# Performance work log

Measured on AMD Instinct MI355X. Metric: run time of the kernel, lower is better.

## Reference

```python
import jax, jax.numpy as jnp
import numpy as np

N = 50000
IN_F = 256
HID = 32
HEADS = 4
NEG_SLOPE = 0.2


def _gat_layer(x, edge_index, W, a_src, a_dst, bias):
    # x: [N, Fin]; W: [Fin, H*C]; a_src/a_dst: [H, C]; bias: [H*C]
    n = x.shape[0]
    H, C = a_src.shape
    h = (x @ W).reshape(n, H, C)                     # [N, H, C]
    alpha_src = jnp.einsum('nhc,hc->nh', h, a_src)   # [N, H]
    alpha_dst = jnp.einsum('nhc,hc->nh', h, a_dst)   # [N, H]
    src, dst = edge_index[0], edge_index[1]
    logits = alpha_src[src] + alpha_dst[dst]         # [E, H]
    logits = jax.nn.leaky_relu(logits, negative_slope=NEG_SLOPE)
    # segment softmax over edges grouped by destination node
    seg_max = jax.ops.segment_max(logits, dst, num_segments=n)
    seg_max = jnp.where(jnp.isfinite(seg_max), seg_max, 0.0)
    e = jnp.exp(logits - seg_max[dst])               # [E, H]
    denom = jax.ops.segment_sum(e, dst, num_segments=n)  # [N, H]
    attn = e / (denom[dst] + 1e-16)                  # [E, H]
    msg = h[src] * attn[:, :, None]                  # [E, H, C]
    out = jax.ops.segment_sum(msg, dst, num_segments=n)  # [N, H, C]
    return out.reshape(n, H * C) + bias


def _add_self_loops(edge_index, n):
    # PyG GATConv default add_self_loops=True
    loops = jnp.arange(n, dtype=edge_index.dtype)
    return jnp.concatenate([edge_index, jnp.stack([loops, loops])], axis=1)


def setup_inputs() -> dict:
    key = jax.random.key(0)
    ks = jax.random.split(key, 10)
    x = jax.random.normal(ks[0], (N, IN_F), dtype=jnp.float32)
    edge_index = jax.random.randint(ks[1], (2, 800000), 0, N, dtype=jnp.int64)
    d1 = HEADS * HID
    s1 = 1.0 / np.sqrt(IN_F)
    W1 = jax.random.normal(ks[2], (IN_F, d1), dtype=jnp.float32) * s1
    a_src1 = jax.random.normal(ks[3], (HEADS, HID), dtype=jnp.float32) * 0.1
    a_dst1 = jax.random.normal(ks[4], (HEADS, HID), dtype=jnp.float32) * 0.1
    b1 = jnp.zeros((d1,), dtype=jnp.float32)
    s2 = 1.0 / np.sqrt(d1)
    W2 = jax.random.normal(ks[5], (d1, d1), dtype=jnp.float32) * s2
    a_src2 = jax.random.normal(ks[6], (HEADS, HID), dtype=jnp.float32) * 0.1
    a_dst2 = jax.random.normal(ks[7], (HEADS, HID), dtype=jnp.float32) * 0.1
    b2 = jnp.zeros((d1,), dtype=jnp.float32)
    return {"x": x, "edge_index": edge_index, "W1": W1, "a_src1": a_src1,
            "a_dst1": a_dst1, "b1": b1, "W2": W2, "a_src2": a_src2,
            "a_dst2": a_dst2, "b2": b2}


def reference(x, edge_index, W1, a_src1, a_dst1, b1, W2, a_src2, a_dst2, b2):
    # Inference mode: dropout layers are identity.
    ei = _add_self_loops(edge_index, x.shape[0])
    h = _gat_layer(x, ei, W1, a_src1, a_dst1, b1)
    h = jax.nn.elu(h)
    h = _gat_layer(h, ei, W2, a_src2, a_dst2, b2)
    return h
```

## Files before the change

kernel.cpp:

```cpp
#include <hip/hip_runtime.h>
#include <hip/hip_fp16.h>
#include <math.h>

#define HEADS 4
#define HID 32
#define D1 128
#define IN_FEAT 256
#define NEG_SLOPE 0.2f
#define CAP 64
#define AGG_NODES 8
#define NPASS 8
#define EPT 8

#define WTS_STRIDE_H 72
#define HTS_STRIDE_H 136
#define SMEM_BYTES (128 * 272)

typedef _Float16 half8 __attribute__((ext_vector_type(8)));
typedef float f32x4 __attribute__((ext_vector_type(4)));
typedef long long ll2 __attribute__((ext_vector_type(2)));

static inline int ceil_div(int a, int b) { return (a + b - 1) / b; }

static __device__ inline float2 unpack_h2(unsigned int v) {
    __half2 h = __builtin_bit_cast(__half2, v);
    return __half22float2(h);
}

static __device__ inline void fma_mix_lo(float& a, unsigned int h2, float w) {
    asm("v_fma_mix_f32 %0, %1, %2, %0 op_sel:[0,0,0] op_sel_hi:[1,0,0]"
        : "+v"(a) : "v"(h2), "v"(w));
}
static __device__ inline void fma_mix_hi(float& a, unsigned int h2, float w) {
    asm("v_fma_mix_f32 %0, %1, %2, %0 op_sel:[1,0,0] op_sel_hi:[1,0,0]"
        : "+v"(a) : "v"(h2), "v"(w));
}

__global__ void init_prep(const unsigned int* __restrict__ raw, int* __restrict__ flag,
                          const float* __restrict__ W1, _Float16* __restrict__ WT1,
                          const float* __restrict__ W2, _Float16* __restrict__ WT2,
                          int* __restrict__ cnt, int N) {
    int i = blockIdx.x * blockDim.x + threadIdx.x;
    if (i < N) cnt[i] = 0;
    if (i < IN_FEAT * D1) {
        int k = i >> 7, n = i & 127;
        WT1[(size_t)n * IN_FEAT + k] = (_Float16)W1[i];
    }
    if (i < D1 * D1) {
        int k = i >> 7, n = i & 127;
        WT2[(size_t)n * D1 + k] = (_Float16)W2[i];
    }
    if (blockIdx.x == 0 && threadIdx.x < 64) {
        unsigned int hi = raw[2 * threadIdx.x + 1];
        unsigned long long b = __ballot(hi != 0u);
        if (threadIdx.x == 0) *flag = (b == 0ULL) ? 1 : 0;
    }
}

__device__ void scatter_body(int sbid, const void* __restrict__ raw,
                             const int* __restrict__ flag,
                             int* __restrict__ cnt,
                             unsigned short* __restrict__ slots,
                             int E, int N) {
    const int e0 = (sbid * 256 + (int)threadIdx.x) * EPT;
    const bool wide = (*flag != 0);
    int s[EPT], d[EPT];
    bool val[EPT];
    if (e0 + EPT <= E) {
        if (wide) {
            const ll2* ps = (const ll2*)((const long long*)raw + e0);
            const ll2* pd = (const ll2*)((const long long*)raw + E + e0);
#pragma unroll
            for (int i = 0; i < EPT / 2; ++i) {
                ll2 a = ps[i], b = pd[i];
                s[2 * i] = (int)a[0]; s[2 * i + 1] = (int)a[1];
                d[2 * i] = (int)b[0]; d[2 * i + 1] = (int)b[1];
            }
        } else {
            const int4* ps = (const int4*)((const int*)raw + e0);
            const int4* pd = (const int4*)((const int*)raw + E + e0);
#pragma unroll
            for (int i = 0; i < EPT / 4; ++i) {
                int4 a = ps[i], b = pd[i];
                s[4 * i] = a.x; s[4 * i + 1] = a.y; s[4 * i + 2] = a.z; s[4 * i + 3] = a.w;
                d[4 * i] = b.x; d[4 * i + 1] = b.y; d[4 * i + 2] = b.z; d[4 * i + 3] = b.w;
            }
        }
#pragma unroll
        for (int i = 0; i < EPT; ++i) val[i] = true;
    } else {
#pragma unroll
        for (int i = 0; i < EPT; ++i) {
            int e = e0 + i;
            val[i] = (e < E);
            if (val[i]) {
                if (wide) { s[i] = (int)((const long long*)raw)[e]; d[i] = (int)((const long long*)raw)[E + e]; }
                else      { s[i] = ((const int*)raw)[e];            d[i] = ((const int*)raw)[E + e]; }
            } else { s[i] = 0; d[i] = -1; }
        }
    }

    const int range = (N + NPASS - 1) / NPASS;
    int lo = 0;
    for (int p = 0; p < NPASS; ++p, lo += range) {
        const int hi = lo + range;
#pragma unroll
        for (int i = 0; i < EPT; ++i) {
            if (val[i] && d[i] >= lo && d[i] < hi) {
                int pos = atomicAdd(&cnt[d[i]], 1);
                if (pos < CAP) slots[(size_t)d[i] * CAP + pos] = (unsigned short)s[i];
            }
        }
        __syncthreads();
    }
}

template <int AF16>
__device__ void gemm_body(char* smem, int bid, const void* __restrict__ Ain,
                          const _Float16* __restrict__ WT,
                          _Float16* __restrict__ Hout,
                          const float* __restrict__ a_src,
                          const float* __restrict__ a_dst,
                          float* __restrict__ asrc_out,
                          float* __restrict__ adst_out,
                          int M, int K) {
    const int tid = threadIdx.x;
    const int wave = tid >> 6, lane = tid & 63;
    const int quad = lane >> 4, l16 = lane & 15;
    const int row0 = bid * 128;
    const int m0 = min(row0 + wave * 32 + l16, M - 1);
    const int m1 = min(row0 + wave * 32 + 16 + l16, M - 1);
    const float*    Af = (const float*)Ain;
    const _Float16* Ah = (const _Float16*)Ain;
    const uint4* WTg = (const uint4*)WT;
    const int K8 = K >> 3;

    f32x4 acc[2][8];
#pragma unroll
    for (int r = 0; r < 2; ++r)
#pragma unroll
        for (int c = 0; c < 8; ++c) acc[r][c] = (f32x4){0.f, 0.f, 0.f, 0.f};

    for (int kb = 0; kb < K; kb += 64) {
        __syncthreads();
#pragma unroll
        for (int i = 0; i < 4; ++i) {
            int c = tid + i * 256;
            int n = c >> 3, j = c & 7;
            uint4 v = WTg[(size_t)n * K8 + (kb >> 3) + j];
            *(uint4*)(smem + n * 144 + j * 16) = v;
        }
        __syncthreads();
#pragma unroll
        for (int kc = 0; kc < 2; ++kc) {
            int k0 = kb + kc * 32 + quad * 8;
            half8 a0f, a1f;
            if (AF16) {
                a0f = *(const half8*)(Ah + (size_t)m0 * K + k0);
                a1f = *(const half8*)(Ah + (size_t)m1 * K + k0);
            } else {
                float4 x0 = *(const float4*)(Af + (size_t)m0 * K + k0);
                float4 x1 = *(const float4*)(Af + (size_t)m0 * K + k0 + 4);
                float4 y0 = *(const float4*)(Af + (size_t)m1 * K + k0);
                float4 y1 = *(const float4*)(Af + (size_t)m1 * K + k0 + 4);
                a0f[0] = (_Float16)x0.x; a0f[1] = (_Float16)x0.y;
                a0f[2] = (_Float16)x0.z; a0f[3] = (_Float16)x0.w;
                a0f[4] = (_Float16)x1.x; a0f[5] = (_Float16)x1.y;
                a0f[6] = (_Float16)x1.z; a0f[7] = (_Float16)x1.w;
                a1f[0] = (_Float16)y0.x; a1f[1] = (_Float16)y0.y;
                a1f[2] = (_Float16)y0.z; a1f[3] = (_Float16)y0.w;
                a1f[4] = (_Float16)y1.x; a1f[5] = (_Float16)y1.y;
                a1f[6] = (_Float16)y1.z; a1f[7] = (_Float16)y1.w;
            }
#pragma unroll
            for (int c = 0; c < 8; ++c) {
                half8 bf = *(const half8*)(smem + (c * 16 + l16) * 144 + kc * 64 + quad * 16);
                acc[0][c] = __builtin_amdgcn_mfma_f32_16x16x32_f16(a0f, bf, acc[0][c], 0, 0, 0);
                acc[1][c] = __builtin_amdgcn_mfma_f32_16x16x32_f16(a1f, bf, acc[1][c], 0, 0, 0);
            }
        }
    }

    __syncthreads();
    _Float16* hts = (_Float16*)smem;
#pragma unroll
    for (int r = 0; r < 2; ++r)
#pragma unroll
        for (int c = 0; c < 8; ++c)
#pragma unroll
            for (int g = 0; g < 4; ++g) {
                int row = wave * 32 + r * 16 + quad * 4 + g;
                hts[row * HTS_STRIDE_H + c * 16 + l16] = (_Float16)acc[r][c][g];
            }
    __syncthreads();

    const int r = tid >> 1;
    const int part = tid & 1;
    const int grow = row0 + r;
    const uint4* hrow = (const uint4*)(smem + r * 272 + part * 128);
    if (grow < M) {
        uint4* dv = (uint4*)(Hout + (size_t)grow * 128 + part * 64);
#pragma unroll
        for (int i = 0; i < 8; ++i) dv[i] = hrow[i];
    }
#pragma unroll
    for (int t = 0; t < 2; ++t) {
        int hh = part * 2 + t;
        const uint4* hv = (const uint4*)(smem + r * 272 + hh * 64);
        const float4* as4 = (const float4*)(a_src + hh * HID);
        const float4* ad4 = (const float4*)(a_dst + hh * HID);
        float ps = 0.f, pd = 0.f;
#pragma unroll
        for (int b = 0; b < 4; ++b) {
            uint4 u = hv[b];
            float2 f0 = unpack_h2(u.x), f1 = unpack_h2(u.y);
            float2 f2 = unpack_h2(u.z), f3 = unpack_h2(u.w);
            float4 s0 = as4[b * 2], s1 = as4[b * 2 + 1];
            float4 d0 = ad4[b * 2], d1 = ad4[b * 2 + 1];
            ps += f0.x * s0.x + f0.y * s0.y + f1.x * s0.z + f1.y * s0.w
                + f2.x * s1.x + f2.y * s1.y + f3.x * s1.z + f3.y * s1.w;
            pd += f0.x * d0.x + f0.y * d0.y + f1.x * d0.z + f1.y * d0.w
                + f2.x * d1.x + f2.y * d1.y + f3.x * d1.z + f3.y * d1.w;
        }
        if (grow < M) {
            asrc_out[grow * 4 + hh] = ps;
            adst_out[grow * 4 + hh] = pd;
        }
    }
}

template <int AF16>
__global__ __launch_bounds__(256) void gemm128(const void* __restrict__ Ain,
                                               const _Float16* __restrict__ WT,
                                               _Float16* __restrict__ Hout,
                                               const float* __restrict__ a_src,
                                               const float* __restrict__ a_dst,
                                               float* __restrict__ asrc_out,
                                               float* __restrict__ adst_out,
                                               int M, int K) {
    __shared__ __align__(16) char smem[SMEM_BYTES];
    gemm_body<AF16>(smem, blockIdx.x, Ain, WT, Hout, a_src, a_dst,
                    asrc_out, adst_out, M, K);
}

template <int AF16>
__global__ __launch_bounds__(256) void gemm128_scatter(const void* __restrict__ Ain,
                                                       const _Float16* __restrict__ WT,
                                                       _Float16* __restrict__ Hout,
                                                       const float* __restrict__ a_src,
                                                       const float* __restrict__ a_dst,
                                                       float* __restrict__ asrc_out,
                                                       float* __restrict__ adst_out,
                                                       int M, int K,
                                                       const void* __restrict__ raw,
                                                       const int* __restrict__ flag,
                                                       int* __restrict__ cnt,
                                                       unsigned short* __restrict__ slots,
                                                       int E, int Sg) {
    __shared__ __align__(16) char smem[SMEM_BYTES];
    if ((int)blockIdx.x < Sg) {
        scatter_body(blockIdx.x, raw, flag, cnt, slots, E, M);
        return;
    }
    gemm_body<AF16>(smem, blockIdx.x - Sg, Ain, WT, Hout, a_src, a_dst,
                    asrc_out, adst_out, M, K);
}

__global__ __launch_bounds__(256) void aggregate(const _Float16* __restrict__ hb,
                                                 const int* __restrict__ cnt,
                                                 const unsigned short* __restrict__ slots,
                                                 const float* __restrict__ asrc,
                                                 const float* __restrict__ adst,
                                                 const float* __restrict__ bias,
                                                 float* __restrict__ out32,
                                                 _Float16* __restrict__ out16,
                                                 int N, int apply_elu) {
    const int w = threadIdx.x >> 6;
    const int lane = threadIdx.x & 63;
    const int half = lane >> 5;
    const int hl = lane & 31;
    const int idx = w * 2 + half;
    const int node = blockIdx.x * AGG_NODES + idx;
    const bool live = (node < N);

    __shared__ float wsh[AGG_NODES][CAP][4];
    __shared__ int ssh[AGG_NODES][CAP];

    int cntE = 0, count = 1;
    if (live) {
        cntE = min(cnt[node], CAP - 1);
        count = cntE + 1;
    }
    const unsigned short* nslots = slots + (size_t)node * CAP;

    float4 ad4 = live ? *(const float4*)&adst[node * 4] : make_float4(0.f, 0.f, 0.f, 0.f);

    const bool v0 = live && (hl < count);
    const bool v1 = live && (hl + 32 < count);
    float lv0[4] = {-1e30f, -1e30f, -1e30f, -1e30f};
    float lv1[4] = {-1e30f, -1e30f, -1e30f, -1e30f};
    if (v0) {
        int src = (hl < cntE) ? (int)nslots[hl] : node;
        ssh[idx][hl] = src << 8;
        float4 as4 = *(const float4*)&asrc[src * 4];
        float t0 = as4.x + ad4.x, t1 = as4.y + ad4.y;
        float t2 = as4.z + ad4.z, t3 = as4.w + ad4.w;
        lv0[0] = t0 > 0.f ? t0 : NEG_SLOPE * t0;
        lv0[1] = t1 > 0.f ? t1 : NEG_SLOPE * t1;
        lv0[2] = t2 > 0.f ? t2 : NEG_SLOPE * t2;
        lv0[3] = t3 > 0.f ? t3 : NEG_SLOPE * t3;
    }
    if (v1) {
        int j = hl + 32;
        int src = (j < cntE) ? (int)nslots[j] : node;
        ssh[idx][j] = src << 8;
        float4 as4 = *(const float4*)&asrc[src * 4];
        float t0 = as4.x + ad4.x, t1 = as4.y + ad4.y;
        float t2 = as4.z + ad4.z, t3 = as4.w + ad4.w;
        lv1[0] = t0 > 0.f ? t0 : NEG_SLOPE * t0;
        lv1[1] = t1 > 0.f ? t1 : NEG_SLOPE * t1;
        lv1[2] = t2 > 0.f ? t2 : NEG_SLOPE * t2;
        lv1[3] = t3 > 0.f ? t3 : NEG_SLOPE * t3;
    }

    float m[4];
#pragma unroll
    for (int h = 0; h < 4; ++h) m[h] = fmaxf(lv0[h], lv1[h]);
#pragma unroll
    for (int off = 16; off >= 1; off >>= 1)
#pragma unroll
        for (int h = 0; h < 4; ++h)
            m[h] = fmaxf(m[h], __shfl_xor(m[h], off, 64));

    float e0[4], e1[4], sum[4];
#pragma unroll
    for (int h = 0; h < 4; ++h) {
        e0[h] = v0 ? __expf(lv0[h] - m[h]) : 0.f;
        e1[h] = v1 ? __expf(lv1[h] - m[h]) : 0.f;
        sum[h] = e0[h] + e1[h];
    }
#pragma unroll
    for (int off = 16; off >= 1; off >>= 1)
#pragma unroll
        for (int h = 0; h < 4; ++h)
            sum[h] += __shfl_xor(sum[h], off, 64);

    if (v0) {
        float4 w4;
        w4.x = e0[0] / (sum[0] + 1e-16f);
        w4.y = e0[1] / (sum[1] + 1e-16f);
        w4.z = e0[2] / (sum[2] + 1e-16f);
        w4.w = e0[3] / (sum[3] + 1e-16f);
        *(float4*)&wsh[idx][hl][0] = w4;
    }
    if (v1) {
        float4 w4;
        w4.x = e1[0] / (sum[0] + 1e-16f);
        w4.y = e1[1] / (sum[1] + 1e-16f);
        w4.z = e1[2] / (sum[2] + 1e-16f);
        w4.w = e1[3] / (sum[3] + 1e-16f);
        *(float4*)&wsh[idx][hl + 32][0] = w4;
    }
    __syncthreads();

    const int q = hl >> 4;
    const int sub = hl & 15;
    const int hh = sub >> 2;
    const char* hbase = (const char*)hb;
    const int sub16 = sub * 16;

    float acc[8];
#pragma unroll
    for (int i = 0; i < 8; ++i) acc[i] = 0.f;

#define LDROW(off) (*(const uint4*)(hbase + (unsigned)((off) + sub16)))
#define ROW_FMA(u, wt)                                   \
    do {                                                 \
        fma_mix_lo(acc[0], (u).x, (wt));                 \
        fma_mix_hi(acc[1], (u).x, (wt));                 \
        fma_mix_lo(acc[2], (u).y, (wt));                 \
        fma_mix_hi(acc[3], (u).y, (wt));                 \
        fma_mix_lo(acc[4], (u).z, (wt));                 \
        fma_mix_hi(acc[5], (u).z, (wt));                 \
        fma_mix_lo(acc[6], (u).w, (wt));                 \
        fma_mix_hi(acc[7], (u).w, (wt));                 \
    } while (0)

    if (live) {
        int j = q;
        if (j + 6 < count) {
            int o0 = ssh[idx][j], o1 = ssh[idx][j + 2], o2 = ssh[idx][j + 4], o3 = ssh[idx][j + 6];
            float w0 = wsh[idx][j][hh], w1 = wsh[idx][j + 2][hh];
            float w2 = wsh[idx][j + 4][hh], w3 = wsh[idx][j + 6][hh];
            uint4 u0 = LDROW(o0), u1 = LDROW(o1), u2 = LDROW(o2), u3 = LDROW(o3);
            for (j += 8; j + 6 < count; j += 8) {
                int p0 = ssh[idx][j], p1 = ssh[idx][j + 2], p2 = ssh[idx][j + 4], p3 = ssh[idx][j + 6];
                float x0 = wsh[idx][j][hh], x1 = wsh[idx][j + 2][hh];
                float x2 = wsh[idx][j + 4][hh], x3 = wsh[idx][j + 6][hh];
                uint4 n0 = LDROW(p0), n1 = LDROW(p1), n2 = LDROW(p2), n3 = LDROW(p3);
                ROW_FMA(u0, w0); ROW_FMA(u1, w1); ROW_FMA(u2, w2); ROW_FMA(u3, w3);
                u0 = n0; u1 = n1; u2 = n2; u3 = n3;
                w0 = x0; w1 = x1; w2 = x2; w3 = x3;
            }
            const bool b0 = j < count, b1 = j + 2 < count, b2 = j + 4 < count;
            uint4 t0 = {0, 0, 0, 0}, t1 = {0, 0, 0, 0}, t2 = {0, 0, 0, 0};
            float y0 = 0.f, y1 = 0.f, y2 = 0.f;
            if (b0) { t0 = LDROW(ssh[idx][j]);     y0 = wsh[idx][j][hh]; }
            if (b1) { t1 = LDROW(ssh[idx][j + 2]); y1 = wsh[idx][j + 2][hh]; }
            if (b2) { t2 = LDROW(ssh[idx][j + 4]); y2 = wsh[idx][j + 4][hh]; }
            ROW_FMA(u0, w0); ROW_FMA(u1, w1); ROW_FMA(u2, w2); ROW_FMA(u3, w3);
            if (b0) ROW_FMA(t0, y0);
            if (b1) ROW_FMA(t1, y1);
            if (b2) ROW_FMA(t2, y2);
        } else {
            const bool b0 = j < count, b1 = j + 2 < count, b2 = j + 4 < count;
            uint4 t0 = {0, 0, 0, 0}, t1 = {0, 0, 0, 0}, t2 = {0, 0, 0, 0};
            float y0 = 0.f, y1 = 0.f, y2 = 0.f;
            if (b0) { t0 = LDROW(ssh[idx][j]);     y0 = wsh[idx][j][hh]; }
            if (b1) { t1 = LDROW(ssh[idx][j + 2]); y1 = wsh[idx][j + 2][hh]; }
            if (b2) { t2 = LDROW(ssh[idx][j + 4]); y2 = wsh[idx][j + 4][hh]; }
            if (b0) ROW_FMA(t0, y0);
            if (b1) ROW_FMA(t1, y1);
            if (b2) ROW_FMA(t2, y2);
        }
    }
#undef ROW_FMA
#undef LDROW

#pragma unroll
    for (int i = 0; i < 8; ++i) acc[i] += __shfl_xor(acc[i], 16, 64);

    if (live && q == 0) {
        int ch8 = sub * 8;
        float o[8];
#pragma unroll
        for (int i = 0; i < 8; ++i) o[i] = acc[i] + bias[ch8 + i];
        if (apply_elu) {
#pragma unroll
            for (int i = 0; i < 8; ++i) o[i] = o[i] > 0.f ? o[i] : __expf(o[i]) - 1.f;
        }
        if (out16) {
            __align__(16) _Float16 t[8];
#pragma unroll
            for (int i = 0; i < 8; ++i) t[i] = (_Float16)o[i];
            *(uint4*)&out16[(size_t)node * D1 + ch8] = *(const uint4*)t;
        } else {
            *(float4*)&out32[(size_t)node * D1 + ch8]     = make_float4(o[0], o[1], o[2], o[3]);
            *(float4*)&out32[(size_t)node * D1 + ch8 + 4] = make_float4(o[4], o[5], o[6], o[7]);
        }
    }
}

extern "C" void kernel_launch(void* const* d_in, const int* in_sizes, int n_in,
                              void* d_out, int out_size, void* d_ws, size_t ws_size,
                              hipStream_t stream) {
    const float* x      = (const float*)d_in[0];
    const void*  e_raw  = d_in[1];
    const float* W1     = (const float*)d_in[2];
    const float* a_src1 = (const float*)d_in[3];
    const float* a_dst1 = (const float*)d_in[4];
    const float* b1     = (const float*)d_in[5];
    const float* W2     = (const float*)d_in[6];
    const float* a_src2 = (const float*)d_in[7];
    const float* a_dst2 = (const float*)d_in[8];
    const float* b2     = (const float*)d_in[9];

    const int N  = in_sizes[0] / IN_FEAT;
    const int E  = in_sizes[1] / 2;
    float* out = (float*)d_out;

    char* ws = (char*)d_ws;
    size_t woff = 0;
    auto walloc = [&](size_t bytes) -> char* {
        char* p = ws + woff;
        woff = (woff + bytes + 255) & ~(size_t)255;
        return p;
    };
    int*   flag  = (int*)walloc(4);
    int*   cnt   = (int*)walloc((size_t)N * 4);
    unsigned short* slots = (unsigned short*)walloc((size_t)N * CAP * 2);
    float* asrc  = (float*)walloc((size_t)N * HEADS * 4);
    float* adst  = (float*)walloc((size_t)N * HEADS * 4);
    _Float16* hb  = (_Float16*)walloc((size_t)N * D1 * 2);
    _Float16* o16 = (_Float16*)walloc((size_t)N * D1 * 2);
    _Float16* WT1 = (_Float16*)walloc((size_t)IN_FEAT * D1 * 2);
    _Float16* WT2 = (_Float16*)walloc((size_t)D1 * D1 * 2);

    const int Gg = ceil_div(N, 128);
    const int Sg = ceil_div(E, 256 * EPT);
    const int Ga = ceil_div(N, AGG_NODES);
    const int initN = (N > IN_FEAT * D1) ? N : IN_FEAT * D1;

    init_prep<<<ceil_div(initN, 256), 256, 0, stream>>>(
        (const unsigned int*)e_raw, flag, W1, WT1, W2, WT2, cnt, N);
    gemm128_scatter<0><<<Sg + Gg, 256, 0, stream>>>(
        x, WT1, hb, a_src1, a_dst1, asrc, adst, N, IN_FEAT,
        e_raw, flag, cnt, slots, E, Sg);
    aggregate<<<Ga, 256, 0, stream>>>(hb, cnt, slots, asrc, adst, b1, nullptr, o16, N, 1);
    gemm128<1><<<Gg, 256, 0, stream>>>(o16, WT2, hb, a_src2, a_dst2, asrc, adst, N, D1);
    aggregate<<<Ga, 256, 0, stream>>>(hb, cnt, slots, asrc, adst, b2, out, nullptr, N, 0);
}
```

Before: 244.1 us.

## Single-pass scatter with fewer edges per thread and halved GEMM epilogue LDS

```diff
diff --git a/kernel.cpp b/kernel.cpp
--- a/kernel.cpp
+++ b/kernel.cpp
@@ -9,12 +9,9 @@
 #define NEG_SLOPE 0.2f
 #define CAP 64
 #define AGG_NODES 8
-#define NPASS 8
-#define EPT 8
-
-#define WTS_STRIDE_H 72
-#define HTS_STRIDE_H 136
-#define SMEM_BYTES (128 * 272)
+#define EPT 4
+
+#define SMEM_BYTES (128 * 144)
 
 typedef _Float16 half8 __attribute__((ext_vector_type(8)));
 typedef float f32x4 __attribute__((ext_vector_type(4)));
@@ -61,57 +58,38 @@
                              const int* __restrict__ flag,
                              int* __restrict__ cnt,
                              unsigned short* __restrict__ slots,
-                             int E, int N) {
+                             int E) {
     const int e0 = (sbid * 256 + (int)threadIdx.x) * EPT;
+    if (e0 >= E) return;
     const bool wide = (*flag != 0);
-    int s[EPT], d[EPT];
-    bool val[EPT];
-    if (e0 + EPT <= E) {
+    int s[4], d[4];
+    if (e0 + 4 <= E) {
         if (wide) {
             const ll2* ps = (const ll2*)((const long long*)raw + e0);
             const ll2* pd = (const ll2*)((const long long*)raw + E + e0);
-#pragma unroll
-            for (int i = 0; i < EPT / 2; ++i) {
-                ll2 a = ps[i], b = pd[i];
-                s[2 * i] = (int)a[0]; s[2 * i + 1] = (int)a[1];
-                d[2 * i] = (int)b[0]; d[2 * i + 1] = (int)b[1];
-            }
+            ll2 a = ps[0], b = ps[1], c = pd[0], e = pd[1];
+            s[0] = (int)a[0]; s[1] = (int)a[1]; s[2] = (int)b[0]; s[3] = (int)b[1];
+            d[0] = (int)c[0]; d[1] = (int)c[1]; d[2] = (int)e[0]; d[3] = (int)e[1];
         } else {
-            const int4* ps = (const int4*)((const int*)raw + e0);
-            const int4* pd = (const int4*)((const int*)raw + E + e0);
-#pragma unroll
-            for (int i = 0; i < EPT / 4; ++i) {
-                int4 a = ps[i], b = pd[i];
-                s[4 * i] = a.x; s[4 * i + 1] = a.y; s[4 * i + 2] = a.z; s[4 * i + 3] = a.w;
-                d[4 * i] = b.x; d[4 * i + 1] = b.y; d[4 * i + 2] = b.z; d[4 * i + 3] = b.w;
-            }
-        }
-#pragma unroll
-        for (int i = 0; i < EPT; ++i) val[i] = true;
+            int4 a = *(const int4*)((const int*)raw + e0);
+            int4 b = *(const int4*)((const int*)raw + E + e0);
+            s[0] = a.x; s[1] = a.y; s[2] = a.z; s[3] = a.w;
+            d[0] = b.x; d[1] = b.y; d[2] = b.z; d[3] = b.w;
+        }
+        int p[4];
+#pragma unroll
+        for (int i = 0; i < 4; ++i) p[i] = atomicAdd(&cnt[d[i]], 1);
+#pragma unroll
+        for (int i = 0; i < 4; ++i)
+            if (p[i] < CAP) slots[(size_t)d[i] * CAP + p[i]] = (unsigned short)s[i];
     } else {
-#pragma unroll
-        for (int i = 0; i < EPT; ++i) {
-            int e = e0 + i;
-            val[i] = (e < E);
-            if (val[i]) {
-                if (wide) { s[i] = (int)((const long long*)raw)[e]; d[i] = (int)((const long long*)raw)[E + e]; }
-                else      { s[i] = ((const int*)raw)[e];            d[i] = ((const int*)raw)[E + e]; }
-            } else { s[i] = 0; d[i] = -1; }
-        }
-    }
-
-    const int range = (N + NPASS - 1) / NPASS;
-    int lo = 0;
-    for (int p = 0; p < NPASS; ++p, lo += range) {
-        const int hi = lo + range;
-#pragma unroll
-        for (int i = 0; i < EPT; ++i) {
-            if (val[i] && d[i] >= lo && d[i] < hi) {
-                int pos = atomicAdd(&cnt[d[i]], 1);
-                if (pos < CAP) slots[(size_t)d[i] * CAP + pos] = (unsigned short)s[i];
-            }
-        }
-        __syncthreads();
+        for (int e = e0; e < E; ++e) {
+            int ss, dd;
+            if (wide) { ss = (int)((const long long*)raw)[e]; dd = (int)((const long long*)raw)[E + e]; }
+            else      { ss = ((const int*)raw)[e];            dd = ((const int*)raw)[E + e]; }
+            int p = atomicAdd(&cnt[dd], 1);
+            if (p < CAP) slots[(size_t)dd * CAP + p] = (unsigned short)ss;
+        }
     }
 }
 
@@ -181,40 +159,37 @@
         }
     }
 
-    __syncthreads();
-    _Float16* hts = (_Float16*)smem;
-#pragma unroll
-    for (int r = 0; r < 2; ++r)
-#pragma unroll
-        for (int c = 0; c < 8; ++c)
-#pragma unroll
-            for (int g = 0; g < 4; ++g) {
-                int row = wave * 32 + r * 16 + quad * 4 + g;
-                hts[row * HTS_STRIDE_H + c * 16 + l16] = (_Float16)acc[r][c][g];
-            }
-    __syncthreads();
-
-    const int r = tid >> 1;
-    const int part = tid & 1;
-    const int grow = row0 + r;
-    const uint4* hrow = (const uint4*)(smem + r * 272 + part * 128);
-    if (grow < M) {
-        uint4* dv = (uint4*)(Hout + (size_t)grow * 128 + part * 64);
-#pragma unroll
-        for (int i = 0; i < 8; ++i) dv[i] = hrow[i];
-    }
-#pragma unroll
-    for (int t = 0; t < 2; ++t) {
-        int hh = part * 2 + t;
-        const uint4* hv = (const uint4*)(smem + r * 272 + hh * 64);
-        const float4* as4 = (const float4*)(a_src + hh * HID);
-        const float4* ad4 = (const float4*)(a_dst + hh * HID);
+    const int lr  = tid >> 2;
+    const int seg = tid & 3;
+    const float4* as4 = (const float4*)(a_src + seg * HID);
+    const float4* ad4 = (const float4*)(a_dst + seg * HID);
+#pragma unroll
+    for (int c = 0; c < 2; ++c) {
+        __syncthreads();
+        if ((wave >> 1) == c) {
+            const int wl = (wave & 1) * 32;
+#pragma unroll
+            for (int r = 0; r < 2; ++r)
+#pragma unroll
+                for (int cc = 0; cc < 8; ++cc)
+#pragma unroll
+                    for (int g = 0; g < 4; ++g) {
+                        int row = wl + r * 16 + quad * 4 + g;
+                        *(_Float16*)(smem + row * 272 + (cc * 16 + l16) * 2) =
+                            (_Float16)acc[r][cc][g];
+                    }
+        }
+        __syncthreads();
+        const int grow = row0 + c * 64 + lr;
+        uint4 u[4];
+#pragma unroll
+        for (int i = 0; i < 4; ++i)
+            u[i] = *(const uint4*)(smem + lr * 272 + seg * 64 + i * 16);
         float ps = 0.f, pd = 0.f;
 #pragma unroll
         for (int b = 0; b < 4; ++b) {
-            uint4 u = hv[b];
-            float2 f0 = unpack_h2(u.x), f1 = unpack_h2(u.y);
-            float2 f2 = unpack_h2(u.z), f3 = unpack_h2(u.w);
+            float2 f0 = unpack_h2(u[b].x), f1 = unpack_h2(u[b].y);
+            float2 f2 = unpack_h2(u[b].z), f3 = unpack_h2(u[b].w);
             float4 s0 = as4[b * 2], s1 = as4[b * 2 + 1];
             float4 d0 = ad4[b * 2], d1 = ad4[b * 2 + 1];
             ps += f0.x * s0.x + f0.y * s0.y + f1.x * s0.z + f1.y * s0.w
@@ -223,8 +198,11 @@
                 + f2.x * d1.x + f2.y * d1.y + f3.x * d1.z + f3.y * d1.w;
         }
         if (grow < M) {
-            asrc_out[grow * 4 + hh] = ps;
-            adst_out[grow * 4 + hh] = pd;
+            uint4* dv = (uint4*)(Hout + (size_t)grow * 128 + seg * 32);
+#pragma unroll
+            for (int i = 0; i < 4; ++i) dv[i] = u[i];
+            asrc_out[grow * 4 + seg] = ps;
+            adst_out[grow * 4 + seg] = pd;
         }
     }
 }
@@ -259,7 +237,7 @@
                                                        int E, int Sg) {
     __shared__ __align__(16) char smem[SMEM_BYTES];
     if ((int)blockIdx.x < Sg) {
-        scatter_body(blockIdx.x, raw, flag, cnt, slots, E, M);
+        scatter_body(blockIdx.x, raw, flag, cnt, slots, E);
         return;
     }
     gemm_body<AF16>(smem, blockIdx.x - Sg, Ain, WT, Hout, a_src, a_dst,
```

Measured after the change: 249.4 us. 2.1% more time.
